# Optimization experiments

Measured on AMD Instinct MI355X. Metric: run time of the kernel, lower is better.

The kernel has to match this reference:

```python
import jax, jax.numpy as jnp
import numpy as np

EMB = 1024
HEADS = 16
HEAD_DIM = EMB // HEADS
FF = 4 * EMB
B, S = 4, 2048


def gelu_tanh(x):
    c = jnp.sqrt(jnp.asarray(2.0 / jnp.pi, x.dtype))
    return 0.5 * x * (1.0 + jnp.tanh(c * (x + 0.044715 * x ** 3)))


def layernorm(x, g, b, eps=1e-5):
    mu = jnp.mean(x, axis=-1, keepdims=True)
    var = jnp.var(x, axis=-1, keepdims=True)
    return (x - mu) * jax.lax.rsqrt(var + eps) * g + b


def setup_inputs() -> dict:
    key = jax.random.key(0)
    ks = jax.random.split(key, 12)
    s = 0.02
    return {
        "x": jax.random.normal(ks[0], (B, S, EMB), jnp.float32),
        "Wq": jax.random.normal(ks[1], (EMB, EMB), jnp.float32) * s,
        "bq": jnp.zeros((EMB,), jnp.float32),
        "Wk": jax.random.normal(ks[2], (EMB, EMB), jnp.float32) * s,
        "bk": jnp.zeros((EMB,), jnp.float32),
        "Wv": jax.random.normal(ks[3], (EMB, EMB), jnp.float32) * s,
        "bv": jnp.zeros((EMB,), jnp.float32),
        "Wo": jax.random.normal(ks[4], (EMB, EMB), jnp.float32) * s,
        "bo": jnp.zeros((EMB,), jnp.float32),
        "W1": jax.random.normal(ks[5], (EMB, FF), jnp.float32) * s,
        "b1": jnp.zeros((FF,), jnp.float32),
        "W2": jax.random.normal(ks[6], (FF, EMB), jnp.float32) * s,
        "b2": jnp.zeros((EMB,), jnp.float32),
        "g1": jnp.ones((EMB,), jnp.float32),
        "be1": jnp.zeros((EMB,), jnp.float32),
        "g2": jnp.ones((EMB,), jnp.float32),
        "be2": jnp.zeros((EMB,), jnp.float32),
    }


def reference(x, Wq, bq, Wk, bk, Wv, bv, Wo, bo, W1, b1, W2, b2, g1, be1, g2, be2):
    b, s, _ = x.shape
    shortcut = x
    h = layernorm(x, g1, be1)
    # QKV projections -> [b, heads, s, head_dim]
    def proj(W, bias):
        return (h @ W + bias).reshape(b, s, HEADS, HEAD_DIM).transpose(0, 2, 1, 3)
    q, k, v = proj(Wq, bq), proj(Wk, bk), proj(Wv, bv)
    scores = jnp.einsum('bhqd,bhkd->bhqk', q, k) / jnp.sqrt(jnp.asarray(HEAD_DIM, x.dtype))
    causal = jnp.triu(jnp.ones((s, s), bool), k=1)  # True above diagonal -> masked
    scores = jnp.where(causal, -jnp.inf, scores)
    probs = jax.nn.softmax(scores, axis=-1)  # dropout p=0 -> identity
    ctx = jnp.einsum('bhqk,bhkd->bhqd', probs, v).transpose(0, 2, 1, 3).reshape(b, s, EMB)
    attn_out = ctx @ Wo + bo
    x = attn_out + shortcut
    shortcut = x
    h = layernorm(x, g2, be2)
    ff = gelu_tanh(h @ W1 + b1) @ W2 + b2
    return ff + shortcut
```

## Files before the change

### kernel.cpp

```cpp
#include <hip/hip_runtime.h>
#include <hip/hip_bf16.h>

#define EMB 1024
#define HEADS 16
#define HDIM 64
#define FFDIM 4096
#define BSZ 4
#define SEQ 2048
#define MROWS (BSZ * SEQ)
#define QKVW 3072
#define VSTRIDE 2080

typedef __attribute__((ext_vector_type(8))) short bf16x8;
typedef __attribute__((ext_vector_type(4))) float f32x4;
typedef __attribute__((ext_vector_type(16))) float f32x16;
typedef __attribute__((ext_vector_type(4))) unsigned short u16x4;
typedef unsigned short u16;

__device__ __forceinline__ float bf2f(u16 u) {
  union { unsigned int i; float f; } c; c.i = ((unsigned int)u) << 16; return c.f;
}
__device__ __forceinline__ u16 f2bf(float f) {
  union { float f; unsigned int i; } c; c.f = f;
  unsigned int i = c.i + 0x7fff + ((c.i >> 16) & 1);
  return (u16)(i >> 16);
}
__device__ __forceinline__ unsigned fbits(float f) {
  union { float f; unsigned u; } c; c.f = f; return c.u;
}
__device__ __forceinline__ unsigned pk2(float e0, float e1) {
  return (fbits(e0) >> 16) | (fbits(e1) & 0xffff0000u);
}
__device__ __forceinline__ f32x16 zero16() {
  f32x16 z;
#pragma unroll
  for (int i = 0; i < 16; ++i) z[i] = 0.f;
  return z;
}
__device__ __forceinline__ void gload16(const u16* g, void* lds) {
  __builtin_amdgcn_global_load_lds(
      (const __attribute__((address_space(1))) void*)g,
      (__attribute__((address_space(3))) void*)lds, 16, 0, 0);
}

__global__ __launch_bounds__(256) void ln_kernel(
    const float* __restrict__ x, const float* __restrict__ g,
    const float* __restrict__ be, u16* __restrict__ out) {
  int w = threadIdx.x >> 6, l = threadIdx.x & 63;
  size_t row = (size_t)blockIdx.x * 4 + w;
  const float* xr = x + row * EMB;
  float f[4][4];
  float s = 0.f, s2 = 0.f;
#pragma unroll
  for (int c = 0; c < 4; ++c) {
    f32x4 v = *(const f32x4*)(xr + c * 256 + l * 4);
#pragma unroll
    for (int j = 0; j < 4; ++j) {
      f[c][j] = v[j];
      s += v[j];
      s2 += v[j] * v[j];
    }
  }
#pragma unroll
  for (int m = 1; m < 64; m <<= 1) {
    s  += __shfl_xor(s, m);
    s2 += __shfl_xor(s2, m);
  }
  float mu = s * (1.f / EMB);
  float var = s2 * (1.f / EMB) - mu * mu;
  float rs = rsqrtf(var + 1e-5f);
#pragma unroll
  for (int c = 0; c < 4; ++c) {
    u16x4 o;
#pragma unroll
    for (int j = 0; j < 4; ++j) {
      int col = c * 256 + l * 4 + j;
      o[j] = f2bf((f[c][j] - mu) * rs * g[col] + be[col]);
    }
    *(u16x4*)(out + row * EMB + c * 256 + l * 4) = o;
  }
}

__global__ __launch_bounds__(256) void transpose_cvt(
    const float* __restrict__ in, u16* __restrict__ out, int R, int C) {
  __shared__ u16 tile[32][33];
  int c0 = blockIdx.x * 32, r0 = blockIdx.y * 32;
  int tx = threadIdx.x, ty = threadIdx.y;
#pragma unroll
  for (int i = ty; i < 32; i += 8)
    tile[i][tx] = f2bf(in[(size_t)(r0 + i) * C + c0 + tx]);
  __syncthreads();
#pragma unroll
  for (int i = ty; i < 32; i += 8)
    out[(size_t)(c0 + i) * R + r0 + tx] = tile[tx][i];
}

__global__ __launch_bounds__(256) void concat_bias(
    const float* __restrict__ a, const float* __restrict__ b,
    const float* __restrict__ c, float* __restrict__ o) {
  int i = blockIdx.x * 256 + threadIdx.x;
  o[i] = i < 1024 ? a[i] : (i < 2048 ? b[i - 1024] : c[i - 2048]);
}

__global__ __launch_bounds__(256) void transpose_v(
    const u16* __restrict__ QKV, u16* __restrict__ Vt) {
  __shared__ u16 tile[32][33];
  int s0 = blockIdx.x * 32, d0 = blockIdx.y * 32, bh = blockIdx.z;
  int h = bh % HEADS, b = bh / HEADS;
  int tx = threadIdx.x, ty = threadIdx.y;
  const u16* src = QKV + (size_t)b * SEQ * QKVW + 2048 + h * HDIM;
  u16* dst = Vt + (size_t)bh * HDIM * VSTRIDE;
#pragma unroll
  for (int i = ty; i < 32; i += 8)
    tile[i][tx] = src[(size_t)(s0 + i) * QKVW + d0 + tx];
  __syncthreads();
#pragma unroll
  for (int i = ty; i < 32; i += 8)
    dst[(size_t)(d0 + i) * VSTRIDE + s0 + tx] = tile[tx][i];
}

__device__ __forceinline__ float gelu_f(float v) {
  float u = 1.5957691216057308f * (v + 0.044715f * v * v * v);
  return v / (1.f + __expf(-u));
}

template <int EPI, typename OT>
__global__ __launch_bounds__(256, 3) void gemm32(
    const u16* __restrict__ A, const u16* __restrict__ Bt,
    const float* __restrict__ bias, const float* __restrict__ res,
    OT* __restrict__ C, int N, int K) {
  __shared__ char lds[32768];
  char* ldsA = lds;
  char* ldsB = lds + 16384;
  int nbn = N >> 7;
  int cpx = gridDim.x >> 3;
  int bid = blockIdx.x;
  int logical = (bid & 7) * cpx + (bid >> 3);
  int mb = logical / nbn, nb = logical % nbn;
  int m0 = mb << 7, n0 = nb << 7;
  int t = threadIdx.x, w = t >> 6, l = t & 63;
  int wr = w >> 1, wc = w & 1;
  int l31 = l & 31, lh = l >> 5;
  int srow8 = l >> 3, sp8 = l & 7;

  f32x16 acc[2][2] = {{zero16(), zero16()}, {zero16(), zero16()}};

  for (int k0 = 0; k0 < K; k0 += 64) {
    __syncthreads();
#pragma unroll
    for (int ps = 0; ps < 4; ++ps) {
      int r = ps * 32 + (w << 3) + srow8;
      int sc = (sp8 ^ (r & 7)) << 3;
      gload16(A + (size_t)(m0 + r) * K + k0 + sc, ldsA + ps * 4096 + (w << 10));
      gload16(Bt + (size_t)(n0 + r) * K + k0 + sc, ldsB + ps * 4096 + (w << 10));
    }
    __syncthreads();
#pragma unroll
    for (int hf = 0; hf < 2; ++hf) {
      bf16x8 afr[2][2], bfr[2][2];
#pragma unroll
      for (int blk = 0; blk < 2; ++blk)
#pragma unroll
        for (int kk = 0; kk < 2; ++kk) {
          int kki = hf * 2 + kk;
          int ra = (wr << 6) + (blk << 5) + l31;
          int rb = (wc << 6) + (blk << 5) + l31;
          int pa = (((kki << 1) + lh) ^ (ra & 7)) << 4;
          int pb = (((kki << 1) + lh) ^ (rb & 7)) << 4;
          afr[blk][kk] = *(const bf16x8*)(ldsA + ra * 128 + pa);
          bfr[blk][kk] = *(const bf16x8*)(ldsB + rb * 128 + pb);
        }
#pragma unroll
      for (int m = 0; m < 2; ++m)
#pragma unroll
        for (int n = 0; n < 2; ++n)
#pragma unroll
          for (int kk = 0; kk < 2; ++kk)
            acc[m][n] = __builtin_amdgcn_mfma_f32_32x32x16_bf16(
                afr[m][kk], bfr[n][kk], acc[m][n], 0, 0, 0);
    }
  }

#pragma unroll
  for (int m = 0; m < 2; ++m)
#pragma unroll
    for (int n = 0; n < 2; ++n) {
      int col = n0 + (wc << 6) + (n << 5) + l31;
      float bcol = bias[col];
      int rbase = m0 + (wr << 6) + (m << 5) + (lh << 2);
#pragma unroll
      for (int reg = 0; reg < 16; ++reg) {
        int row = rbase + (reg & 3) + ((reg >> 2) << 3);
        float v = acc[m][n][reg] + bcol;
        if (EPI & 2) v = gelu_f(v);
        if (EPI & 1) v += res[(size_t)row * N + col];
        if (sizeof(OT) == 2)
          C[(size_t)row * N + col] = (OT)f2bf(v);
        else
          C[(size_t)row * N + col] = (OT)v;
      }
    }
}

#define QKT(ACCS, QF)                                                       \
  do {                                                                      \
    ACCS = zero16();                                                        \
    _Pragma("unroll") for (int s_ = 0; s_ < 4; ++s_)                        \
        ACCS = __builtin_amdgcn_mfma_f32_32x32x16_bf16(kf[s_], QF[s_],      \
                                                       ACCS, 0, 0, 0);      \
  } while (0)

#define STEP(ACCS, L, O0, O1, DIAG)                                         \
  do {                                                                      \
    float e_[16];                                                           \
    _Pragma("unroll") for (int i = 0; i < 16; ++i) {                        \
      float sv = ACCS[i];                                                   \
      if (DIAG) {                                                           \
        int kvl = (i & 3) + 8 * (i >> 2) + 4 * g;                           \
        if (kvl > lq) sv = -1e30f;                                          \
      }                                                                     \
      e_[i] = __expf(sv);                                                   \
    }                                                                       \
    float ts = 0.f;                                                         \
    _Pragma("unroll") for (int i = 0; i < 16; ++i) ts += e_[i];             \
    ts += __shfl_xor(ts, 32);                                               \
    L += ts;                                                                \
    _Pragma("unroll") for (int s_ = 0; s_ < 2; ++s_) {                      \
      unsigned plo0 = pk2(e_[8 * s_ + 0], e_[8 * s_ + 1]);                  \
      unsigned plo1 = pk2(e_[8 * s_ + 2], e_[8 * s_ + 3]);                  \
      unsigned phi0 = pk2(e_[8 * s_ + 4], e_[8 * s_ + 5]);                  \
      unsigned phi1 = pk2(e_[8 * s_ + 6], e_[8 * s_ + 7]);                  \
      unsigned recv0 = __shfl_xor(g ? plo0 : phi0, 32);                     \
      unsigned recv1 = __shfl_xor(g ? plo1 : phi1, 32);                     \
      union { unsigned u[4]; bf16x8 v; } pf_;                               \
      pf_.u[0] = g ? recv0 : plo0;                                          \
      pf_.u[1] = g ? recv1 : plo1;                                          \
      pf_.u[2] = g ? phi0 : recv0;                                          \
      pf_.u[3] = g ? phi1 : recv1;                                          \
      O0 = __builtin_amdgcn_mfma_f32_32x32x16_bf16(vf0[s_], pf_.v, O0,      \
                                                   0, 0, 0);                \
      O1 = __builtin_amdgcn_mfma_f32_32x32x16_bf16(vf1[s_], pf_.v, O1,      \
                                                   0, 0, 0);                \
    }                                                                       \
  } while (0)

#define LOADKV(KV0)                                                         \
  do {                                                                      \
    _Pragma("unroll") for (int s_ = 0; s_ < 4; ++s_)                        \
        kf[s_] = *(const bf16x8*)(Kp + (size_t)((KV0) + lq) * QKVW +        \
                                  s_ * 16 + g * 8);                         \
    _Pragma("unroll") for (int s_ = 0; s_ < 2; ++s_) {                      \
      vf0[s_] = *(const bf16x8*)(Vt + (size_t)lq * VSTRIDE + (KV0) +        \
                                 s_ * 16 + g * 8);                          \
      vf1[s_] = *(const bf16x8*)(Vt + (size_t)(32 + lq) * VSTRIDE +         \
                                 (KV0) + s_ * 16 + g * 8);                  \
    }                                                                       \
  } while (0)

#define WRITE_OUT(O0, O1, L, WQ0)                                           \
  do {                                                                      \
    float inv = 1.f / L;                                                    \
    u16* orow = Op + (size_t)((WQ0) + lq) * EMB;                            \
    _Pragma("unroll") for (int dblk = 0; dblk < 2; ++dblk) {                \
      _Pragma("unroll") for (int p = 0; p < 8; ++p) {                       \
        int i0 = 2 * p;                                                     \
        int d = dblk * 32 + 2 * (p & 1) + 8 * (p >> 1) + 4 * g;             \
        float v0 = (dblk ? O1[i0] : O0[i0]) * inv;                          \
        float v1 = (dblk ? O1[i0 + 1] : O0[i0 + 1]) * inv;                  \
        unsigned wd = (unsigned)f2bf(v0) | ((unsigned)f2bf(v1) << 16);      \
        *(unsigned*)(orow + d) = wd;                                        \
      }                                                                     \
    }                                                                       \
  } while (0)

__global__ __launch_bounds__(256, 2) void attn_kernel(
    const u16* __restrict__ QKV, const u16* __restrict__ VtG,
    u16* __restrict__ O) {
  int t = threadIdx.x, w = t >> 6, l = t & 63;
  int lq = l & 31, g = l >> 5;
  int wid = blockIdx.x * 4 + w;
  int qi = wid & 31, bh = wid >> 5;
  int h = bh & (HEADS - 1), b = bh >> 4;
  int wq0a = qi * 32, wq0b = (63 - qi) * 32;
  int ntA = qi + 1, ntB = 64 - qi;
  const u16* Qp = QKV + (size_t)b * SEQ * QKVW + h * HDIM;
  const u16* Kp = QKV + (size_t)b * SEQ * QKVW + 1024 + h * HDIM;
  const u16* Vt = VtG + (size_t)bh * HDIM * VSTRIDE;
  u16* Op = O + (size_t)b * SEQ * EMB + h * HDIM;

  bf16x8 qfA[4], qfB[4];
#pragma unroll
  for (int s = 0; s < 4; ++s) {
    bf16x8 ra = *(const bf16x8*)(Qp + (size_t)(wq0a + lq) * QKVW + s * 16 + g * 8);
    bf16x8 rb = *(const bf16x8*)(Qp + (size_t)(wq0b + lq) * QKVW + s * 16 + g * 8);
#pragma unroll
    for (int j = 0; j < 8; ++j) {
      qfA[s][j] = (short)f2bf(bf2f((u16)ra[j]) * 0.125f);
      qfB[s][j] = (short)f2bf(bf2f((u16)rb[j]) * 0.125f);
    }
  }

  f32x16 oA0 = zero16(), oA1 = zero16(), oB0 = zero16(), oB1 = zero16();
  f32x16 sA, sB;
  float lA = 0.f, lB = 0.f;
  bf16x8 kf[4], vf0[2], vf1[2];

  for (int ti = 0; ti < ntA; ++ti) {
    LOADKV(ti * 32);
    QKT(sA, qfA);
    QKT(sB, qfB);
    bool diagA = (ti == ntA - 1);
    STEP(sA, lA, oA0, oA1, diagA);
    STEP(sB, lB, oB0, oB1, false);
  }
  WRITE_OUT(oA0, oA1, lA, wq0a);
  for (int ti = ntA; ti < ntB; ++ti) {
    LOADKV(ti * 32);
    QKT(sB, qfB);
    bool diagB = (ti == ntB - 1);
    STEP(sB, lB, oB0, oB1, diagB);
  }
  WRITE_OUT(oB0, oB1, lB, wq0b);
}

extern "C" void kernel_launch(void* const* d_in, const int* in_sizes, int n_in,
                              void* d_out, int out_size, void* d_ws, size_t ws_size,
                              hipStream_t stream) {
  (void)in_sizes; (void)n_in; (void)out_size; (void)ws_size;
  const float* x   = (const float*)d_in[0];
  const float* Wq  = (const float*)d_in[1];
  const float* bq  = (const float*)d_in[2];
  const float* Wk  = (const float*)d_in[3];
  const float* bk  = (const float*)d_in[4];
  const float* Wv  = (const float*)d_in[5];
  const float* bv  = (const float*)d_in[6];
  const float* Wo  = (const float*)d_in[7];
  const float* bo  = (const float*)d_in[8];
  const float* W1  = (const float*)d_in[9];
  const float* b1  = (const float*)d_in[10];
  const float* W2  = (const float*)d_in[11];
  const float* b2  = (const float*)d_in[12];
  const float* g1  = (const float*)d_in[13];
  const float* be1 = (const float*)d_in[14];
  const float* g2  = (const float*)d_in[15];
  const float* be2 = (const float*)d_in[16];

  char* ws = (char*)d_ws;
  const size_t MB = 1ull << 20;
  u16*   WqkvT = (u16*)(ws + 0 * MB);
  u16*   WoT   = (u16*)(ws + 6 * MB);
  u16*   W1T   = (u16*)(ws + 8 * MB);
  u16*   W2T   = (u16*)(ws + 16 * MB);
  float* bqkv  = (float*)(ws + 24 * MB);
  u16*   hbuf  = (u16*)(ws + 25 * MB);
  float* x1f   = (float*)(ws + 41 * MB);
  u16*   qkv   = (u16*)(ws + 73 * MB);
  u16*   VtG   = (u16*)(ws + 121 * MB);
  u16*   gbuf  = (u16*)(ws + 73 * MB);

  dim3 tb(32, 8);
  transpose_cvt<<<dim3(EMB / 32, EMB / 32), tb, 0, stream>>>(Wq, WqkvT, EMB, EMB);
  transpose_cvt<<<dim3(EMB / 32, EMB / 32), tb, 0, stream>>>(Wk, WqkvT + 1024 * 1024, EMB, EMB);
  transpose_cvt<<<dim3(EMB / 32, EMB / 32), tb, 0, stream>>>(Wv, WqkvT + 2 * 1024 * 1024, EMB, EMB);
  transpose_cvt<<<dim3(EMB / 32, EMB / 32), tb, 0, stream>>>(Wo, WoT, EMB, EMB);
  transpose_cvt<<<dim3(FFDIM / 32, EMB / 32), tb, 0, stream>>>(W1, W1T, EMB, FFDIM);
  transpose_cvt<<<dim3(EMB / 32, FFDIM / 32), tb, 0, stream>>>(W2, W2T, FFDIM, EMB);
  concat_bias<<<12, 256, 0, stream>>>(bq, bk, bv, bqkv);

  ln_kernel<<<MROWS / 4, 256, 0, stream>>>(x, g1, be1, hbuf);

  gemm32<0, u16><<<(MROWS / 128) * (QKVW / 128), 256, 0, stream>>>(
      hbuf, WqkvT, bqkv, nullptr, qkv, QKVW, EMB);

  transpose_v<<<dim3(SEQ / 32, HDIM / 32, BSZ * HEADS), tb, 0, stream>>>(qkv, VtG);

  attn_kernel<<<BSZ * HEADS * (SEQ / 64) / 4, 256, 0, stream>>>(qkv, VtG, hbuf);

  gemm32<1, float><<<(MROWS / 128) * (EMB / 128), 256, 0, stream>>>(
      hbuf, WoT, bo, x, x1f, EMB, EMB);

  ln_kernel<<<MROWS / 4, 256, 0, stream>>>(x1f, g2, be2, hbuf);

  gemm32<2, u16><<<(MROWS / 128) * (FFDIM / 128), 256, 0, stream>>>(
      hbuf, W1T, b1, nullptr, gbuf, FFDIM, EMB);
  gemm32<1, float><<<(MROWS / 128) * (EMB / 128), 256, 0, stream>>>(
      gbuf, W2T, b2, x1f, (float*)d_out, EMB, FFDIM);
}
```

Baseline: 446.8 us.

## Double-buffer K/V tiles in per-wave LDS slabs with async loads and MFMA priority

Replaces the direct global-to-register K/V fragment loads in the attention loop with asynchronous global-to-LDS copies (gload16) into a per-wave double-buffered, XOR-swizzled LDS slab, so the next tile is prefetched while the current tile is computed. It also raises wave priority around the MFMA sequences via s_setprio. This aims to hide global memory latency in the attention inner loop, at the cost of 64KB of LDS per block, which may limit occupancy. The explicit vmcnt waits with no wave barrier depend on each wave only touching its own slab.

```diff
diff --git a/kernel.cpp b/kernel.cpp
--- a/kernel.cpp
+++ b/kernel.cpp
@@ -205,9 +205,11 @@
 #define QKT(ACCS, QF)                                                       \
   do {                                                                      \
     ACCS = zero16();                                                        \
+    __builtin_amdgcn_s_setprio(1);                                          \
     _Pragma("unroll") for (int s_ = 0; s_ < 4; ++s_)                        \
         ACCS = __builtin_amdgcn_mfma_f32_32x32x16_bf16(kf[s_], QF[s_],      \
                                                        ACCS, 0, 0, 0);      \
+    __builtin_amdgcn_s_setprio(0);                                          \
   } while (0)
 
 #define STEP(ACCS, L, O0, O1, DIAG)                                         \
@@ -237,23 +239,43 @@
       pf_.u[1] = g ? recv1 : plo1;                                          \
       pf_.u[2] = g ? phi0 : recv0;                                          \
       pf_.u[3] = g ? phi1 : recv1;                                          \
+      __builtin_amdgcn_s_setprio(1);                                        \
       O0 = __builtin_amdgcn_mfma_f32_32x32x16_bf16(vf0[s_], pf_.v, O0,      \
                                                    0, 0, 0);                \
       O1 = __builtin_amdgcn_mfma_f32_32x32x16_bf16(vf1[s_], pf_.v, O1,      \
                                                    0, 0, 0);                \
+      __builtin_amdgcn_s_setprio(0);                                        \
     }                                                                       \
   } while (0)
 
-#define LOADKV(KV0)                                                         \
+#define STAGE(KV0, BUF)                                                     \
   do {                                                                      \
-    _Pragma("unroll") for (int s_ = 0; s_ < 4; ++s_)                        \
-        kf[s_] = *(const bf16x8*)(Kp + (size_t)((KV0) + lq) * QKVW +        \
-                                  s_ * 16 + g * 8);                         \
+    char* sb_ = myslab + (BUF) * 8192;                                      \
+    _Pragma("unroll") for (int i_ = 0; i_ < 4; ++i_) {                      \
+      int r_ = i_ * 8 + (l >> 3);                                           \
+      gload16(Kp + (size_t)((KV0) + r_) * QKVW + (((l & 7) ^ (r_ & 7)) << 3),\
+              sb_ + i_ * 1024);                                             \
+    }                                                                       \
+    _Pragma("unroll") for (int i_ = 0; i_ < 4; ++i_) {                      \
+      int r_ = i_ * 16 + (l >> 2);                                          \
+      gload16(Vt + (size_t)r_ * VSTRIDE + (KV0) + (((l & 3) ^ (r_ & 3)) << 3),\
+              sb_ + 4096 + i_ * 1024);                                      \
+    }                                                                       \
+  } while (0)
+
+#define RDFRAGS(BUF)                                                        \
+  do {                                                                      \
+    const char* sb_ = myslab + (BUF) * 8192;                                \
+    _Pragma("unroll") for (int s_ = 0; s_ < 4; ++s_) {                      \
+      int c_ = s_ * 2 + g;                                                  \
+      kf[s_] = *(const bf16x8*)(sb_ + lq * 128 + ((c_ ^ (lq & 7)) << 4));   \
+    }                                                                       \
     _Pragma("unroll") for (int s_ = 0; s_ < 2; ++s_) {                      \
-      vf0[s_] = *(const bf16x8*)(Vt + (size_t)lq * VSTRIDE + (KV0) +        \
-                                 s_ * 16 + g * 8);                          \
-      vf1[s_] = *(const bf16x8*)(Vt + (size_t)(32 + lq) * VSTRIDE +         \
-                                 (KV0) + s_ * 16 + g * 8);                  \
+      int c_ = s_ * 2 + g;                                                  \
+      vf0[s_] = *(const bf16x8*)(sb_ + 4096 + lq * 64 +                     \
+                                 ((c_ ^ (lq & 3)) << 4));                   \
+      vf1[s_] = *(const bf16x8*)(sb_ + 4096 + (32 + lq) * 64 +              \
+                                 ((c_ ^ (lq & 3)) << 4));                   \
     }                                                                       \
   } while (0)
 
@@ -276,8 +298,10 @@
 __global__ __launch_bounds__(256, 2) void attn_kernel(
     const u16* __restrict__ QKV, const u16* __restrict__ VtG,
     u16* __restrict__ O) {
+  __shared__ char slabs[4][16384];
   int t = threadIdx.x, w = t >> 6, l = t & 63;
   int lq = l & 31, g = l >> 5;
+  char* myslab = slabs[w];
   int wid = blockIdx.x * 4 + w;
   int qi = wid & 31, bh = wid >> 5;
   int h = bh & (HEADS - 1), b = bh >> 4;
@@ -305,8 +329,11 @@
   float lA = 0.f, lB = 0.f;
   bf16x8 kf[4], vf0[2], vf1[2];
 
+  STAGE(0, 0);
   for (int ti = 0; ti < ntA; ++ti) {
-    LOADKV(ti * 32);
+    STAGE((ti + 1) * 32, (ti + 1) & 1);
+    asm volatile("s_waitcnt vmcnt(8)" ::: "memory");
+    RDFRAGS(ti & 1);
     QKT(sA, qfA);
     QKT(sB, qfB);
     bool diagA = (ti == ntA - 1);
@@ -315,7 +342,13 @@
   }
   WRITE_OUT(oA0, oA1, lA, wq0a);
   for (int ti = ntA; ti < ntB; ++ti) {
-    LOADKV(ti * 32);
+    if (ti + 1 < ntB) {
+      STAGE((ti + 1) * 32, (ti + 1) & 1);
+      asm volatile("s_waitcnt vmcnt(8)" ::: "memory");
+    } else {
+      asm volatile("s_waitcnt vmcnt(0)" ::: "memory");
+    }
+    RDFRAGS(ti & 1);
     QKT(sB, qfB);
     bool diagB = (ti == ntB - 1);
     STEP(sB, lB, oB0, oB1, diagB);
```

New measurement: 409.5 us. 8.4% less time.
